# Kernel optimization log

Measured on AMD Instinct MI355X. Metric: run time of the kernel, lower is better.

The kernel has to match this reference:

```python
import jax, jax.numpy as jnp
import numpy as np

B, T, D, A = 32, 4096, 512, 64


def setup_inputs() -> dict:
    key = jax.random.key(0)
    k_x, k_m, k_w1, k_b1, k_w2 = jax.random.split(key, 5)
    x = jax.random.normal(k_x, (B, T, D), dtype=jnp.float32)
    mask = jax.random.randint(k_m, (B, T), 0, 2) > 0
    mask = mask.at[:, 0].set(True)  # guarantee >=1 valid step per row
    # params of attention MLP: Linear(D->A) with bias, Linear(A->1) no bias
    W1 = jax.random.normal(k_w1, (A, D), dtype=jnp.float32) / np.sqrt(D)
    b1 = jax.random.normal(k_b1, (A,), dtype=jnp.float32) * 0.01
    w2 = jax.random.normal(k_w2, (A,), dtype=jnp.float32) / np.sqrt(A)
    return {"x": x, "mask": mask, "W1": W1, "b1": b1, "w2": w2}


def reference(x, mask, W1, b1, w2):
    h = jnp.tanh(jnp.einsum('btd,ad->bta', x, W1) + b1)
    scores = jnp.einsum('bta,a->bt', h, w2)
    scores = jnp.where(mask, scores, -jnp.inf)
    weights = jax.nn.softmax(scores, axis=-1)          # (B, T)
    context = jnp.einsum('bt,btd->bd', weights, x)     # (B, D)
    return context, weights
```

## Files before the change

kernel.cpp:

```cpp
#include <hip/hip_runtime.h>
#include <math.h>

#define NB 32
#define NT 4096
#define ND 512
#define NA 64
#define ND4 (ND / 4)
#define RPB 128
#define NBLK (NB * NT / RPB)
#define NPW (NT / RPB)

typedef __attribute__((ext_vector_type(8))) short short8;
typedef __attribute__((ext_vector_type(4))) float f32x4;

__device__ __forceinline__ uint cvtpk(float f0, float f1) {
    uint r;
    asm("v_cvt_pk_bf16_f32 %0, %1, %2" : "=v"(r) : "v"(f0), "v"(f1));
    return r;
}
__device__ __forceinline__ void split2(float f0, float f1, uint& hw, uint& lw) {
    hw = cvtpk(f0, f1);
    float r0 = f0 - __uint_as_float(hw << 16);
    float r1 = f1 - __uint_as_float(hw & 0xffff0000u);
    lw = cvtpk(r0, r1);
}
__device__ __forceinline__ void split8(float4 a, float4 b, short8& hi, short8& lo) {
    union U { short8 s; uint u[4]; } H, L;
    split2(a.x, a.y, H.u[0], L.u[0]);
    split2(a.z, a.w, H.u[1], L.u[1]);
    split2(b.x, b.y, H.u[2], L.u[2]);
    split2(b.z, b.w, H.u[3], L.u[3]);
    hi = H.s; lo = L.s;
}

__device__ __forceinline__ float fast_tanh(float z) {
    z = fminf(fmaxf(z, -15.f), 15.f);
    float t = __expf(2.f * z);
    return (t - 1.f) * __builtin_amdgcn_rcpf(t + 1.f);
}

__global__ __launch_bounds__(256) void k_prep(
    const float* __restrict__ W1, short8* __restrict__ whi, short8* __restrict__ wlo)
{
    int t = blockIdx.x * 256 + threadIdx.x;
    int l  = t & 63;
    int nt = (t >> 6) & 3;
    int ks = t >> 8;
    int a  = nt * 16 + (l & 15);
    int kb = ks * 32 + (l >> 4) * 8;
    const float* p = W1 + a * ND + kb;
    float4 u = *(const float4*)p;
    float4 v = *(const float4*)(p + 4);
    short8 hi, lo;
    split8(u, v, hi, lo);
    whi[t] = hi;
    wlo[t] = lo;
}

__global__ __launch_bounds__(256, 4) void k_fused(
    const float* __restrict__ x, const int* __restrict__ mask,
    const short8* __restrict__ whi, const short8* __restrict__ wlo,
    const float* __restrict__ b1, const float* __restrict__ w2,
    float* __restrict__ escore, float* __restrict__ pctx, float* __restrict__ pden)
{
    __shared__ float ctxl[4][ND];
    __shared__ float wlx[4];

    const int tid = threadIdx.x;
    const int wv  = tid >> 6;
    const int l   = tid & 63;
    const int lr  = l & 15;
    const int lq  = l >> 4;
    const size_t row0 = (size_t)blockIdx.x * RPB + (size_t)wv * 32;

    const float4* __restrict__ x4 = reinterpret_cast<const float4*>(x);
    const float* xb = x + (row0 + lr) * ND + lq * 8;

    float w2v[4], b1v[4];
#pragma unroll
    for (int nt = 0; nt < 4; ++nt) {
        w2v[nt] = w2[nt * 16 + lr];
        b1v[nt] = b1[nt * 16 + lr];
    }

    f32x4 acc[2][4];
#pragma unroll
    for (int mt = 0; mt < 2; ++mt)
#pragma unroll
        for (int nt = 0; nt < 4; ++nt) acc[mt][nt] = (f32x4)0.f;

    for (int ks = 0; ks < 16; ++ks) {
        short8 ahi[2], alo[2];
#pragma unroll
        for (int mt = 0; mt < 2; ++mt) {
            const float* p = xb + mt * 16 * ND + ks * 32;
            float4 u = *(const float4*)p;
            float4 v = *(const float4*)(p + 4);
            split8(u, v, ahi[mt], alo[mt]);
        }
#pragma unroll
        for (int nt = 0; nt < 4; ++nt) {
            short8 bh = whi[(ks * 4 + nt) * 64 + l];
            short8 bl = wlo[(ks * 4 + nt) * 64 + l];
#pragma unroll
            for (int mt = 0; mt < 2; ++mt) {
                acc[mt][nt] = __builtin_amdgcn_mfma_f32_16x16x32_bf16(ahi[mt], bh, acc[mt][nt], 0, 0, 0);
                acc[mt][nt] = __builtin_amdgcn_mfma_f32_16x16x32_bf16(ahi[mt], bl, acc[mt][nt], 0, 0, 0);
                acc[mt][nt] = __builtin_amdgcn_mfma_f32_16x16x32_bf16(alo[mt], bh, acc[mt][nt], 0, 0, 0);
            }
        }
    }

    float ev[2][4];
#pragma unroll
    for (int mt = 0; mt < 2; ++mt) {
#pragma unroll
        for (int rg = 0; rg < 4; ++rg) {
            float s = 0.f;
#pragma unroll
            for (int nt = 0; nt < 4; ++nt)
                s += w2v[nt] * fast_tanh(acc[mt][nt][rg] + b1v[nt]);
            s += __shfl_xor(s, 1);
            s += __shfl_xor(s, 2);
            s += __shfl_xor(s, 4);
            s += __shfl_xor(s, 8);
            int ridx = mt * 16 + lq * 4 + rg;
            bool valid = (mask[row0 + ridx] != 0);
            float e = valid ? __expf(s) : 0.f;
            if (lr == 0) escore[row0 + ridx] = e;
            ev[mt][rg] = e;
        }
    }

    float wl = (ev[0][0] + ev[0][1]) + (ev[0][2] + ev[0][3])
             + (ev[1][0] + ev[1][1]) + (ev[1][2] + ev[1][3]);
    wl += __shfl_xor(wl, 16);
    wl += __shfl_xor(wl, 32);
    if (l == 0) wlx[wv] = wl;

    float4 ca = {0.f, 0.f, 0.f, 0.f}, cb = {0.f, 0.f, 0.f, 0.f};
#pragma unroll
    for (int t = 0; t < 32; ++t) {
        float e = __shfl(ev[t >> 4][t & 3], ((t >> 2) & 3) * 16);
        float4 xa = x4[(row0 + t) * ND4 + l];
        float4 xv = x4[(row0 + t) * ND4 + 64 + l];
        ca.x = fmaf(e, xa.x, ca.x);
        ca.y = fmaf(e, xa.y, ca.y);
        ca.z = fmaf(e, xa.z, ca.z);
        ca.w = fmaf(e, xa.w, ca.w);
        cb.x = fmaf(e, xv.x, cb.x);
        cb.y = fmaf(e, xv.y, cb.y);
        cb.z = fmaf(e, xv.z, cb.z);
        cb.w = fmaf(e, xv.w, cb.w);
    }

    *(float4*)&ctxl[wv][4 * l]       = ca;
    *(float4*)&ctxl[wv][256 + 4 * l] = cb;
    __syncthreads();

    float s0 = (ctxl[0][tid] + ctxl[1][tid]) + (ctxl[2][tid] + ctxl[3][tid]);
    int t2 = tid + 256;
    float s1 = (ctxl[0][t2] + ctxl[1][t2]) + (ctxl[2][t2] + ctxl[3][t2]);
    pctx[(size_t)blockIdx.x * ND + tid] = s0;
    pctx[(size_t)blockIdx.x * ND + t2]  = s1;
    if (tid == 0)
        pden[blockIdx.x] = (wlx[0] + wlx[1]) + (wlx[2] + wlx[3]);
}

__global__ __launch_bounds__(256) void k_tail(
    const float* __restrict__ pctx, const float* __restrict__ pden,
    const float* __restrict__ escore,
    float* __restrict__ ctx, float* __restrict__ weights)
{
    int bid = blockIdx.x, tid = threadIdx.x;
    if (bid < NB) {
        int b = bid;
        float denom = 0.f;
        for (int i = 0; i < NPW; ++i) denom += pden[b * NPW + i];
        float inv = 1.f / denom;
        int d0 = 2 * tid;
        float a0 = 0.f, a1 = 0.f;
        for (int i = 0; i < NPW; ++i) {
            a0 += pctx[(size_t)(b * NPW + i) * ND + d0];
            a1 += pctx[(size_t)(b * NPW + i) * ND + d0 + 1];
        }
        ctx[(size_t)b * ND + d0]     = a0 * inv;
        ctx[(size_t)b * ND + d0 + 1] = a1 * inv;
    } else {
        int i = (bid - NB) * 256 + tid;
        int b = i >> 12;
        float denom = 0.f;
        for (int j = 0; j < NPW; ++j) denom += pden[b * NPW + j];
        weights[i] = escore[i] * (1.f / denom);
    }
}

extern "C" void kernel_launch(void* const* d_in, const int* in_sizes, int n_in,
                              void* d_out, int out_size, void* d_ws, size_t ws_size,
                              hipStream_t stream)
{
    const float* x    = (const float*)d_in[0];
    const int*   mask = (const int*)d_in[1];
    const float* W1   = (const float*)d_in[2];
    const float* b1   = (const float*)d_in[3];
    const float* w2   = (const float*)d_in[4];

    float* ctx     = (float*)d_out;
    float* weights = (float*)d_out + NB * ND;

    float* ws      = (float*)d_ws;
    float* escore  = ws;
    float* pctx    = ws + NB * NT;
    float* pden    = pctx + (size_t)NBLK * ND;
    short8* whi    = (short8*)(pden + NBLK);
    short8* wlo    = whi + 16 * 4 * 64;

    k_prep<<<16, 256, 0, stream>>>(W1, whi, wlo);
    k_fused<<<NBLK, 256, 0, stream>>>(x, mask, whi, wlo, b1, w2,
                                      escore, pctx, pden);
    k_tail<<<NB + NB * NT / 256, 256, 0, stream>>>(pctx, pden, escore,
                                                   ctx, weights);
}
```

Measured before the change: 94.57 us.

## Split K dimension across wave pairs with LDS reduction in fused kernel

Doubles the block to 512 threads so that two waves share each 32-row group, each computing half of the K=512 reduction with MFMA. The partial accumulators are combined through shared memory, one wave computes scores and exp values, and the context accumulation is split by rows across the pair. The goal is more waves in flight to hide memory latency on x. The cost is extra LDS traffic, two more barriers, and idle half-waves during the score phase.

```diff
diff --git a/kernel.cpp b/kernel.cpp
--- a/kernel.cpp
+++ b/kernel.cpp
@@ -57,24 +57,27 @@
     wlo[t] = lo;
 }
 
-__global__ __launch_bounds__(256, 4) void k_fused(
+__global__ __launch_bounds__(512, 8) void k_fused(
     const float* __restrict__ x, const int* __restrict__ mask,
     const short8* __restrict__ whi, const short8* __restrict__ wlo,
     const float* __restrict__ b1, const float* __restrict__ w2,
     float* __restrict__ escore, float* __restrict__ pctx, float* __restrict__ pden)
 {
-    __shared__ float ctxl[4][ND];
-    __shared__ float wlx[4];
+    __shared__ float pool[8192];
+    __shared__ float evl[4][32];
+    __shared__ float wlxg[4];
 
     const int tid = threadIdx.x;
-    const int wv  = tid >> 6;
+    const int w   = tid >> 6;
+    const int g   = w >> 1;
+    const int h   = w & 1;
     const int l   = tid & 63;
     const int lr  = l & 15;
     const int lq  = l >> 4;
-    const size_t row0 = (size_t)blockIdx.x * RPB + (size_t)wv * 32;
+    const size_t row0 = (size_t)blockIdx.x * RPB + (size_t)g * 32;
 
     const float4* __restrict__ x4 = reinterpret_cast<const float4*>(x);
-    const float* xb = x + (row0 + lr) * ND + lq * 8;
+    const float* xb = x + (row0 + lr) * ND + lq * 8 + h * 256;
 
     float w2v[4], b1v[4];
 #pragma unroll
@@ -89,11 +92,12 @@
 #pragma unroll
         for (int nt = 0; nt < 4; ++nt) acc[mt][nt] = (f32x4)0.f;
 
-    for (int ks = 0; ks < 16; ++ks) {
+    for (int ks8 = 0; ks8 < 8; ++ks8) {
+        const int ks = h * 8 + ks8;
         short8 ahi[2], alo[2];
 #pragma unroll
         for (int mt = 0; mt < 2; ++mt) {
-            const float* p = xb + mt * 16 * ND + ks * 32;
+            const float* p = xb + mt * 16 * ND + ks8 * 32;
             float4 u = *(const float4*)p;
             float4 v = *(const float4*)(p + 4);
             split8(u, v, ahi[mt], alo[mt]);
@@ -111,39 +115,54 @@
         }
     }
 
-    float ev[2][4];
-#pragma unroll
-    for (int mt = 0; mt < 2; ++mt) {
-#pragma unroll
-        for (int rg = 0; rg < 4; ++rg) {
-            float s = 0.f;
-#pragma unroll
-            for (int nt = 0; nt < 4; ++nt)
-                s += w2v[nt] * fast_tanh(acc[mt][nt][rg] + b1v[nt]);
-            s += __shfl_xor(s, 1);
-            s += __shfl_xor(s, 2);
-            s += __shfl_xor(s, 4);
-            s += __shfl_xor(s, 8);
-            int ridx = mt * 16 + lq * 4 + rg;
-            bool valid = (mask[row0 + ridx] != 0);
-            float e = valid ? __expf(s) : 0.f;
-            if (lr == 0) escore[row0 + ridx] = e;
-            ev[mt][rg] = e;
-        }
-    }
-
-    float wl = (ev[0][0] + ev[0][1]) + (ev[0][2] + ev[0][3])
-             + (ev[1][0] + ev[1][1]) + (ev[1][2] + ev[1][3]);
-    wl += __shfl_xor(wl, 16);
-    wl += __shfl_xor(wl, 32);
-    if (l == 0) wlx[wv] = wl;
+    float* af = (float*)acc;
+    if (h == 1) {
+#pragma unroll
+        for (int j = 0; j < 32; ++j) pool[g * 2048 + j * 64 + l] = af[j];
+    }
+    __syncthreads();
+
+    if (h == 0) {
+#pragma unroll
+        for (int j = 0; j < 32; ++j) af[j] += pool[g * 2048 + j * 64 + l];
+
+#pragma unroll
+        for (int mt = 0; mt < 2; ++mt) {
+#pragma unroll
+            for (int rg = 0; rg < 4; ++rg) {
+                float s = 0.f;
+#pragma unroll
+                for (int nt = 0; nt < 4; ++nt)
+                    s += w2v[nt] * fast_tanh(acc[mt][nt][rg] + b1v[nt]);
+                s += __shfl_xor(s, 1);
+                s += __shfl_xor(s, 2);
+                s += __shfl_xor(s, 4);
+                s += __shfl_xor(s, 8);
+                int ridx = mt * 16 + lq * 4 + rg;
+                bool valid = (mask[row0 + ridx] != 0);
+                float e = valid ? __expf(s) : 0.f;
+                if (lr == 0) {
+                    escore[row0 + ridx] = e;
+                    evl[g][ridx] = e;
+                }
+                acc[mt][0][rg] = e;
+            }
+        }
+        float wl = (acc[0][0][0] + acc[0][0][1]) + (acc[0][0][2] + acc[0][0][3])
+                 + (acc[1][0][0] + acc[1][0][1]) + (acc[1][0][2] + acc[1][0][3]);
+        wl += __shfl_xor(wl, 16);
+        wl += __shfl_xor(wl, 32);
+        if (l == 0) wlxg[g] = wl;
+    }
+    __syncthreads();
 
     float4 ca = {0.f, 0.f, 0.f, 0.f}, cb = {0.f, 0.f, 0.f, 0.f};
 #pragma unroll
-    for (int t = 0; t < 32; ++t) {
-        float e = __shfl(ev[t >> 4][t & 3], ((t >> 2) & 3) * 16);
-        float4 xa = x4[(row0 + t) * ND4 + l];
-        float4 xv = x4[(row0 + t) * ND4 + 64 + l];
+    for (int t = 0; t < 16; ++t) {
+        int tt = h * 16 + t;
+        float e = evl[g][tt];
+        float4 xa = x4[(row0 + tt) * ND4 + l];
+        float4 xv = x4[(row0 + tt) * ND4 + 64 + l];
         ca.x = fmaf(e, xa.x, ca.x);
         ca.y = fmaf(e, xa.y, ca.y);
         ca.z = fmaf(e, xa.z, ca.z);
@@ -154,17 +173,16 @@
         cb.w = fmaf(e, xv.w, cb.w);
     }
 
-    *(float4*)&ctxl[wv][4 * l]       = ca;
-    *(float4*)&ctxl[wv][256 + 4 * l] = cb;
+    *(float4*)&pool[w * 512 + 4 * l]       = ca;
+    *(float4*)&pool[w * 512 + 256 + 4 * l] = cb;
     __syncthreads();
 
-    float s0 = (ctxl[0][tid] + ctxl[1][tid]) + (ctxl[2][tid] + ctxl[3][tid]);
-    int t2 = tid + 256;
-    float s1 = (ctxl[0][t2] + ctxl[1][t2]) + (ctxl[2][t2] + ctxl[3][t2]);
+    float s0 = 0.f;
+#pragma unroll
+    for (int ww = 0; ww < 8; ++ww) s0 += pool[ww * 512 + tid];
     pctx[(size_t)blockIdx.x * ND + tid] = s0;
-    pctx[(size_t)blockIdx.x * ND + t2]  = s1;
     if (tid == 0)
-        pden[blockIdx.x] = (wlx[0] + wlx[1]) + (wlx[2] + wlx[3]);
+        pden[blockIdx.x] = (wlxg[0] + wlxg[1]) + (wlxg[2] + wlxg[3]);
 }
 
 __global__ __launch_bounds__(256) void k_tail(
@@ -216,7 +234,7 @@
     short8* wlo    = whi + 16 * 4 * 64;
 
     k_prep<<<16, 256, 0, stream>>>(W1, whi, wlo);
-    k_fused<<<NBLK, 256, 0, stream>>>(x, mask, whi, wlo, b1, w2,
+    k_fused<<<NBLK, 512, 0, stream>>>(x, mask, whi, wlo, b1, w2,
                                       escore, pctx, pden);
     k_tail<<<NB + NB * NT / 256, 256, 0, stream>>>(pctx, pden, escore,
                                                    ctx, weights);
```

Measured after the change: 150.9 us. 59.5% more time.
